# Performance work log

Hardware: AMD Instinct MI355X
Metric: run time of the kernel (lower is better)

## Reference

```python
import jax, jax.numpy as jnp
import numpy as np

# ---- constants derived exactly as in CQCCExtractor.__init__ ----
SR = 16000
FMIN = 32.7
N_BINS = 96
BINS_OCT = 24
N_CQCC = 20
HOP = 128
Q = 1.0 / (2.0 ** (1.0 / BINS_OCT) - 1.0)
MIN_WIN = max(16, int(Q * SR / FMIN))          # 16699
N_FFT = 1
while N_FFT < MIN_WIN * 2:
    N_FFT <<= 1                                # 65536
NUM_FREQ = N_FFT // 2 + 1                      # 32769


def _dct_mat():
    k = np.arange(N_CQCC)[:, None]
    n = np.arange(N_BINS)[None, :]
    return jnp.asarray(np.cos(np.pi * k * (2 * n + 1) / (2 * N_BINS)), dtype=jnp.float32)


def _delta(feat, N=2):
    # vectorized version of the per-frame python loop: d[t] = sum_n n*(f[min(t+n,T-1)] - f[max(t-n,0)]) / denom
    denom = 2 * sum(i * i for i in range(1, N + 1))
    T = feat.shape[0]
    p = jnp.concatenate([jnp.repeat(feat[:1], N, axis=0), feat, jnp.repeat(feat[-1:], N, axis=0)], axis=0)
    num = sum(n * (p[N + n:N + n + T] - p[N - n:N - n + T]) for n in range(1, N + 1))
    return num / denom


def setup_inputs() -> dict:
    key = jax.random.key(0)
    wav = jax.random.normal(key, (262144,), dtype=jnp.float32)
    return {"wav": wav}


def reference(wav) -> jnp.ndarray:
    # periodic hann window of length MIN_WIN, zero-padded (centered) to N_FFT like torch.stft
    w = 0.5 - 0.5 * jnp.cos(2.0 * jnp.pi * jnp.arange(MIN_WIN, dtype=jnp.float32) / MIN_WIN)
    left = (N_FFT - MIN_WIN) // 2
    win = jnp.zeros((N_FFT,), dtype=jnp.float32).at[left:left + MIN_WIN].set(w)

    # torch.stft(center=True, pad_mode='reflect')
    pad = N_FFT // 2
    x = jnp.pad(wav, pad, mode='reflect')
    n_frames = 1 + wav.shape[0] // HOP
    starts = jnp.arange(n_frames) * HOP
    frames = x[starts[:, None] + jnp.arange(N_FFT)[None, :]] * win      # [T, n_fft]
    spec = jnp.fft.rfft(frames, axis=-1)                                 # [T, F] complex64
    power = jnp.abs(spec) ** 2                                           # [T, F]

    # linear interpolation of STFT power at geometrically spaced CQT freqs
    cqt_freqs = FMIN * 2.0 ** (jnp.arange(N_BINS, dtype=jnp.float32) / BINS_OCT)
    idx_float = cqt_freqs / (SR / 2) * (NUM_FREQ - 1)
    idx_lo = jnp.clip(idx_float.astype(jnp.int32), 0, NUM_FREQ - 2)
    idx_hi = idx_lo + 1
    alpha = (idx_float - idx_lo.astype(jnp.float32))                     # [n_bins]
    cqt_power = (1.0 - alpha) * power[:, idx_lo] + alpha * power[:, idx_hi]  # [T, n_bins]

    log_cqt = jnp.log(jnp.maximum(cqt_power, 1e-8))
    cqcc = log_cqt @ _dct_mat().T                                        # [T, n_cqcc]
    # normalize over time (torch.std default is unbiased, ddof=1)
    cqcc = (cqcc - cqcc.mean(axis=0)) / (jnp.std(cqcc, axis=0, ddof=1) + 1e-8)

    d1 = _delta(cqcc)
    d2 = _delta(d1)
    return jnp.concatenate([cqcc, d1, d2], axis=-1)                      # [T, 3*n_cqcc]
```

## Files before the change

### kernel.cpp

```cpp
#include <hip/hip_runtime.h>
#include <math.h>

#define WAV_N     262144
#define HOP       128
#define MIN_WIN   16699
#define LEFT      24418
#define T_FRAMES  2049
#define N_BINS    96
#define N_CQCC    20
#define F_COMP    192
#define NF        576
#define NBLK      2179
#define NBP       2240
#define PARTLEN   59
#define FULLBLK   130
#define XS_VALID  278843

#define BT 64
#define FT 32
#define ASTRIDE 68

#define WS_QFP  0
#define WS_SC   20643840
#define WS_CQ   23801856
#define WS_SUMS 23965776
#define SCP     2056

__device__ __forceinline__ void f_to_fi_sigma(int f, int& fi, int& sigma) {
    int plane = f / 192;
    int c = f - plane * 192;
    int bin = c >> 1, hi = c & 1;
    float e    = (float)bin / 24.0f;
    float fb   = 32.7f * exp2f(e);
    float idxf = fb / 8000.0f * 32768.0f;
    fi = (int)idxf + hi;
    sigma = (plane == 0) ? 0 : (plane == 1 ? 1 : -1);
}

__global__ __launch_bounds__(256) void k_chunk(const float* __restrict__ wav,
                                               float4* __restrict__ QFP) {
    __shared__ float A_lds[128 * ASTRIDE];
    __shared__ __align__(16) float4 E_lds[128 * 16];
    int tid = threadIdx.x;
    int b0 = blockIdx.x * BT;
    int f0 = blockIdx.y * FT;

    {
        int sbase = 128 * b0;
        #pragma unroll
        for (int i = 0; i < 32; ++i) {
            int m = i * 256 + tid;
            int s = sbase + m;
            float v = 0.0f;
            if (s < XS_VALID) {
                int j = s - 8350;
                if (j < 0) j = -j;
                if (j >= WAV_N) j = 2 * WAV_N - 2 - j;
                v = wav[j];
            }
            A_lds[(m & 127) * ASTRIDE + (m >> 7)] = v;
        }
    }
    {
        #pragma unroll
        for (int i = 0; i < 8; ++i) {
            int ii = i * 256 + tid;
            int j = ii >> 4, ftp = ii & 15;
            float4 ev;
            #pragma unroll
            for (int half = 0; half < 2; ++half) {
                int f = f0 + 2 * ftp + half;
                int fi, sg; f_to_fi_sigma(f, fi, sg);
                float fr = (float)((j * fi) & 65535) * (1.0f / 65536.0f)
                         - (float)sg * (float)j * (1.0f / (float)MIN_WIN);
                fr -= rintf(fr);
                float sn, cs;
                __sincosf(6.283185307179586f * fr, &sn, &cs);
                if (half == 0) { ev.x = cs; ev.y = -sn; }
                else           { ev.z = cs; ev.w = -sn; }
            }
            E_lds[ii] = ev;
        }
    }
    __syncthreads();

    int ftp = tid & 15;
    int bg  = tid >> 4;
    float xr0[4] = {0,0,0,0}, xi0[4] = {0,0,0,0};
    float xr1[4] = {0,0,0,0}, xi1[4] = {0,0,0,0};
    float pr0[4], pi0[4], pr1[4], pi1[4];

    #pragma unroll 4
    for (int j = 0; j < PARTLEN; ++j) {
        float4 ev = E_lds[j * 16 + ftp];
        float4 a  = *(const float4*)&A_lds[j * ASTRIDE + bg * 4];
        const float aa[4] = {a.x, a.y, a.z, a.w};
        #pragma unroll
        for (int i = 0; i < 4; ++i) {
            xr0[i] = fmaf(aa[i], ev.x, xr0[i]); xi0[i] = fmaf(aa[i], ev.y, xi0[i]);
            xr1[i] = fmaf(aa[i], ev.z, xr1[i]); xi1[i] = fmaf(aa[i], ev.w, xi1[i]);
        }
    }
    #pragma unroll
    for (int i = 0; i < 4; ++i) {
        pr0[i] = xr0[i]; pi0[i] = xi0[i]; pr1[i] = xr1[i]; pi1[i] = xi1[i];
    }
    #pragma unroll 4
    for (int j = PARTLEN; j < 128; ++j) {
        float4 ev = E_lds[j * 16 + ftp];
        float4 a  = *(const float4*)&A_lds[j * ASTRIDE + bg * 4];
        const float aa[4] = {a.x, a.y, a.z, a.w};
        #pragma unroll
        for (int i = 0; i < 4; ++i) {
            xr0[i] = fmaf(aa[i], ev.x, xr0[i]); xi0[i] = fmaf(aa[i], ev.y, xi0[i]);
            xr1[i] = fmaf(aa[i], ev.z, xr1[i]); xi1[i] = fmaf(aa[i], ev.w, xi1[i]);
        }
    }

    int bBase = b0 + bg * 4;
    #pragma unroll
    for (int half = 0; half < 2; ++half) {
        int f = f0 + 2 * ftp + half;
        int fi, sg; f_to_fi_sigma(f, fi, sg);
        float4* dst = QFP + (size_t)f * NBP + bBase;
        #pragma unroll
        for (int i = 0; i < 4; ++i) {
            int b = bBase + i;
            unsigned ph = ((unsigned)fi * (unsigned)(LEFT + 128 * b)) & 65535u;
            float frf = (float)ph * (1.0f / 65536.0f)
                      - (float)sg * (float)((128 * b) % MIN_WIN) * (1.0f / (float)MIN_WIN);
            frf -= rintf(frf);
            float sn, cs;
            __sincosf(6.283185307179586f * frf, &sn, &cs);
            float fr_ = half ? xr1[i] : xr0[i], fi_ = half ? xi1[i] : xi0[i];
            float gr_ = half ? pr1[i] : pr0[i], gi_ = half ? pi1[i] : pi0[i];
            dst[i] = make_float4(fr_ * cs + fi_ * sn, fi_ * cs - fr_ * sn,
                                 gr_ * cs + gi_ * sn, gi_ * cs - gr_ * sn);
        }
    }
}

#define SEG 9
__global__ __launch_bounds__(256) void k_scan(const float4* __restrict__ QFP,
                                              float2* __restrict__ Sc,
                                              double* __restrict__ sums) {
    __shared__ float4 col[NBLK];
    __shared__ float2 acc[T_FRAMES];
    __shared__ double2 wsum[4];
    int tid = threadIdx.x;
    int c = blockIdx.x;
    if (c == 0 && tid < 40) sums[tid] = 0.0;

    for (int plane = 0; plane < 3; ++plane) {
        int f = plane * 192 + c;
        const float4* g = QFP + (size_t)f * NBP;
        #pragma unroll
        for (int k = 0; k < SEG; ++k) {
            int idx = k * 256 + tid;
            if (idx < NBLK) col[idx] = g[idx];
        }
        __syncthreads();
        int s0 = tid * SEG, s1 = min(s0 + SEG, NBLK);
        double sr = 0.0, si = 0.0;
        for (int i = s0; i < s1; ++i) { sr += col[i].x; si += col[i].y; }
        double r = sr, im = si;
        #pragma unroll
        for (int off = 1; off < 64; off <<= 1) {
            double pr = __shfl_up(r, off);
            double pi = __shfl_up(im, off);
            if ((tid & 63) >= off) { r += pr; im += pi; }
        }
        if ((tid & 63) == 63) wsum[tid >> 6] = make_double2(r, im);
        __syncthreads();
        double basr = 0.0, basi = 0.0;
        int w = tid >> 6;
        for (int ww = 0; ww < w; ++ww) { basr += wsum[ww].x; basi += wsum[ww].y; }
        double gr = basr + r - sr, gi = basi + im - si;
        for (int i = s0; i < s1; ++i) {
            float qx = col[i].x, qy = col[i].y;
            col[i].x = (float)gr; col[i].y = (float)gi;
            gr += qx; gi += qy;
        }
        __syncthreads();
        int fi_, sg_; f_to_fi_sigma(f, fi_, sg_);
        #pragma unroll
        for (int k = 0; k < SEG; ++k) {
            int t = k * 256 + tid;
            if (t < T_FRAMES) {
                float4 ca = col[t];
                float4 cb = col[t + FULLBLK];
                float ur = cb.x - ca.x + cb.z;
                float ui = cb.y - ca.y + cb.w;
                unsigned ph = ((unsigned)fi_ * 128u * (unsigned)t) & 65535u;
                float frf = (float)ph * (1.0f / 65536.0f)
                          - (float)sg_ * (float)((128 * t) % MIN_WIN) * (1.0f / (float)MIN_WIN);
                frf -= rintf(frf);
                float sn, cs;
                __sincosf(6.283185307179586f * frf, &sn, &cs);
                float vr = ur * cs - ui * sn;
                float vi = ur * sn + ui * cs;
                if (plane == 0) acc[t] = make_float2(0.5f * vr, 0.5f * vi);
                else { acc[t].x -= 0.25f * vr; acc[t].y -= 0.25f * vi; }
            }
        }
        __syncthreads();
    }
    #pragma unroll
    for (int k = 0; k < SEG; ++k) {
        int t = k * 256 + tid;
        if (t < T_FRAMES) Sc[(size_t)c * SCP + t] = acc[t];
    }
}

__global__ __launch_bounds__(256) void k_cqt(const float2* __restrict__ Sc,
                                             float* __restrict__ cq,
                                             double* __restrict__ sums) {
    __shared__ float dctm[N_CQCC * N_BINS];
    __shared__ float lg[8][N_BINS];
    __shared__ float cqv[8][N_CQCC];
    int tid = threadIdx.x;
    int tb = blockIdx.x * 8;
    for (int idx = tid; idx < N_CQCC * N_BINS; idx += 256) {
        int k = idx / N_BINS, b = idx - k * N_BINS;
        dctm[idx] = cosf((float)M_PI * (float)(k * (2 * b + 1)) / 192.0f);
    }
    int lt = tid >> 5, lane = tid & 31;
    int t = tb + lt;
    #pragma unroll
    for (int bb = 0; bb < 3; ++bb) {
        int b = lane + 32 * bb;
        float lv = 0.0f;
        if (t < T_FRAMES) {
            float2 lo = Sc[(size_t)(2 * b) * SCP + t];
            float2 hi = Sc[(size_t)(2 * b + 1) * SCP + t];
            float pl = lo.x * lo.x + lo.y * lo.y;
            float ph = hi.x * hi.x + hi.y * hi.y;
            float e    = (float)b / 24.0f;
            float fb   = 32.7f * exp2f(e);
            float idxf = fb / 8000.0f * 32768.0f;
            float alpha = idxf - (float)((int)idxf);
            float p = (1.0f - alpha) * pl + alpha * ph;
            lv = logf(fmaxf(p, 1e-8f));
        }
        lg[lt][b] = lv;
    }
    __syncthreads();
    if (tid < 8 * N_CQCC) {
        int lt2 = tid / N_CQCC, k = tid - lt2 * N_CQCC;
        int t2 = tb + lt2;
        float s = 0.0f;
        #pragma unroll 4
        for (int b = 0; b < N_BINS; ++b) s += dctm[k * N_BINS + b] * lg[lt2][b];
        cqv[lt2][k] = (t2 < T_FRAMES) ? s : 0.0f;
        if (t2 < T_FRAMES) cq[t2 * N_CQCC + k] = s;
    }
    __syncthreads();
    if (tid < N_CQCC) {
        double s1 = 0.0, s2 = 0.0;
        #pragma unroll
        for (int lt2 = 0; lt2 < 8; ++lt2) {
            if (tb + lt2 < T_FRAMES) {
                double v = (double)cqv[lt2][tid];
                s1 += v; s2 += v * v;
            }
        }
        atomicAdd(&sums[tid], s1);
        atomicAdd(&sums[N_CQCC + tid], s2);
    }
}

__device__ __forceinline__ int clampT(int v) {
    return v < 0 ? 0 : (v > T_FRAMES - 1 ? T_FRAMES - 1 : v);
}

__global__ void k_final(const float* __restrict__ cq, const double* __restrict__ sums,
                        float* __restrict__ out) {
    int gid = blockIdx.x * blockDim.x + threadIdx.x;
    if (gid >= T_FRAMES * N_CQCC) return;
    int t = gid / N_CQCC;
    int k = gid - t * N_CQCC;
    double S1 = sums[k], S2 = sums[N_CQCC + k];
    double md = S1 / (double)T_FRAMES;
    double var = (S2 - S1 * md) / (double)(T_FRAMES - 1);
    double sd = sqrt(var > 0.0 ? var : 0.0);
    float m = (float)md;
    float iv = (float)(1.0 / (sd + 1e-8));
    float cv[9];
    #pragma unroll
    for (int j = 0; j < 9; ++j)
        cv[j] = (cq[clampT(t + j - 4) * N_CQCC + k] - m) * iv;
    float dv[5];
    #pragma unroll
    for (int o = -2; o <= 2; ++o) {
        int p = clampT(t + o);
        int h1 = clampT(p + 1) - t, l1 = clampT(p - 1) - t;
        int h2 = clampT(p + 2) - t, l2 = clampT(p - 2) - t;
        dv[o + 2] = ((cv[h1 + 4] - cv[l1 + 4]) + 2.0f * (cv[h2 + 4] - cv[l2 + 4])) * 0.1f;
    }
    out[t * 60 + k]      = cv[4];
    out[t * 60 + 20 + k] = dv[2];
    out[t * 60 + 40 + k] = (dv[3] - dv[1] + 2.0f * (dv[4] - dv[0])) * 0.1f;
}

extern "C" void kernel_launch(void* const* d_in, const int* in_sizes, int n_in,
                              void* d_out, int out_size, void* d_ws, size_t ws_size,
                              hipStream_t stream) {
    const float* wav = (const float*)d_in[0];
    float* out = (float*)d_out;
    char* ws = (char*)d_ws;
    float4* QFP  = (float4*)(ws + WS_QFP);
    float2* Sc   = (float2*)(ws + WS_SC);
    float*  cq   = (float*)(ws + WS_CQ);
    double* sums = (double*)(ws + WS_SUMS);

    k_chunk<<<dim3((NBLK + BT - 1) / BT, NF / FT), 256, 0, stream>>>(wav, QFP);
    k_scan<<<F_COMP, 256, 0, stream>>>(QFP, Sc, sums);
    k_cqt<<<(T_FRAMES + 7) / 8, 256, 0, stream>>>(Sc, cq, sums);
    k_final<<<(T_FRAMES * N_CQCC + 255) / 256, 256, 0, stream>>>(cq, sums, out);
}
```

Measured before the change: 125.0 us.

## Generate chunk twiddles by recurrence and stream samples through LDS in chunks

k_chunk no longer precomputes a table of complex exponentials in shared memory. Each thread now builds them in registers with a complex-rotation recurrence, reseeded with an exact sincos at the start of each 32-sample chunk. Samples are staged in 32-row chunks, and each thread now covers 8 blocks × 2 frequencies, with 64 frequencies per workgroup. The aim is to remove the E table's LDS reads and the sincos setup, raise FMA-per-load reuse and shrink LDS so occupancy can rise. In exchange it adds per-thread register pressure, extra barriers, and accumulated float error from the recurrence across up to 32 steps.

```diff
diff --git a/kernel.cpp b/kernel.cpp
--- a/kernel.cpp
+++ b/kernel.cpp
@@ -15,10 +15,12 @@
 #define PARTLEN   59
 #define FULLBLK   130
 #define XS_VALID  278843
-
-#define BT 64
-#define FT 32
-#define ASTRIDE 68
+#define TWOPI     6.283185307179586f
+
+#define BT   64
+#define FTW  64
+#define JC   32
+#define AST  68
 
 #define WS_QFP  0
 #define WS_SC   20643840
@@ -39,103 +41,102 @@
 
 __global__ __launch_bounds__(256) void k_chunk(const float* __restrict__ wav,
                                                float4* __restrict__ QFP) {
-    __shared__ float A_lds[128 * ASTRIDE];
-    __shared__ __align__(16) float4 E_lds[128 * 16];
+    __shared__ float A_lds[JC * AST];
     int tid = threadIdx.x;
     int b0 = blockIdx.x * BT;
-    int f0 = blockIdx.y * FT;
-
-    {
-        int sbase = 128 * b0;
-        #pragma unroll
-        for (int i = 0; i < 32; ++i) {
+    int f0 = blockIdx.y * FTW;
+    int ftp = tid & 31;
+    int bg  = tid >> 5;
+    int bb  = b0 + bg * 8;
+
+    int fi[2], sg[2];
+    f_to_fi_sigma(f0 + 2 * ftp,     fi[0], sg[0]);
+    f_to_fi_sigma(f0 + 2 * ftp + 1, fi[1], sg[1]);
+
+    float Dr[2], Di[2];
+    #pragma unroll
+    for (int h = 0; h < 2; ++h) {
+        float fr = (float)fi[h] * (1.0f / 65536.0f)
+                 - (float)sg[h] * (1.0f / (float)MIN_WIN);
+        fr -= rintf(fr);
+        float sn, cs; __sincosf(TWOPI * fr, &sn, &cs);
+        Dr[h] = cs; Di[h] = -sn;
+    }
+
+    float xr[2][8], xi[2][8], pr[2][8], pi[2][8];
+    #pragma unroll
+    for (int h = 0; h < 2; ++h)
+        #pragma unroll
+        for (int i = 0; i < 8; ++i) { xr[h][i] = 0.f; xi[h][i] = 0.f; }
+
+    for (int jc = 0; jc < 4; ++jc) {
+        int jbase = jc * JC;
+        __syncthreads();
+        #pragma unroll
+        for (int i = 0; i < 8; ++i) {
             int m = i * 256 + tid;
-            int s = sbase + m;
+            int j = m & 31, bl = m >> 5;
+            int s = 128 * (b0 + bl) + jbase + j;
             float v = 0.0f;
             if (s < XS_VALID) {
-                int j = s - 8350;
-                if (j < 0) j = -j;
-                if (j >= WAV_N) j = 2 * WAV_N - 2 - j;
-                v = wav[j];
-            }
-            A_lds[(m & 127) * ASTRIDE + (m >> 7)] = v;
-        }
-    }
-    {
+                int w = s - 8350;
+                if (w < 0) w = -w;
+                if (w >= WAV_N) w = 2 * WAV_N - 2 - w;
+                v = wav[w];
+            }
+            A_lds[j * AST + bl] = v;
+        }
+        __syncthreads();
+        float Wr[2], Wi[2];
+        #pragma unroll
+        for (int h = 0; h < 2; ++h) {
+            float fr = (float)((jbase * fi[h]) & 65535) * (1.0f / 65536.0f)
+                     - (float)sg[h] * (float)jbase * (1.0f / (float)MIN_WIN);
+            fr -= rintf(fr);
+            float sn, cs; __sincosf(TWOPI * fr, &sn, &cs);
+            Wr[h] = cs; Wi[h] = -sn;
+        }
+        #pragma unroll 8
+        for (int j32 = 0; j32 < JC; ++j32) {
+            if (jc == 1 && j32 == PARTLEN - 32) {
+                #pragma unroll
+                for (int h = 0; h < 2; ++h)
+                    #pragma unroll
+                    for (int i = 0; i < 8; ++i) { pr[h][i] = xr[h][i]; pi[h][i] = xi[h][i]; }
+            }
+            float4 a0 = *(const float4*)&A_lds[j32 * AST + bg * 8];
+            float4 a1 = *(const float4*)&A_lds[j32 * AST + bg * 8 + 4];
+            const float aa[8] = {a0.x, a0.y, a0.z, a0.w, a1.x, a1.y, a1.z, a1.w};
+            #pragma unroll
+            for (int h = 0; h < 2; ++h) {
+                float wr = Wr[h], wi = Wi[h];
+                #pragma unroll
+                for (int i = 0; i < 8; ++i) {
+                    xr[h][i] = fmaf(aa[i], wr, xr[h][i]);
+                    xi[h][i] = fmaf(aa[i], wi, xi[h][i]);
+                }
+                Wr[h] = wr * Dr[h] - wi * Di[h];
+                Wi[h] = wr * Di[h] + wi * Dr[h];
+            }
+        }
+    }
+
+    #pragma unroll
+    for (int h = 0; h < 2; ++h) {
+        int f = f0 + 2 * ftp + h;
+        float4* dst = QFP + (size_t)f * NBP + bb;
         #pragma unroll
         for (int i = 0; i < 8; ++i) {
-            int ii = i * 256 + tid;
-            int j = ii >> 4, ftp = ii & 15;
-            float4 ev;
-            #pragma unroll
-            for (int half = 0; half < 2; ++half) {
-                int f = f0 + 2 * ftp + half;
-                int fi, sg; f_to_fi_sigma(f, fi, sg);
-                float fr = (float)((j * fi) & 65535) * (1.0f / 65536.0f)
-                         - (float)sg * (float)j * (1.0f / (float)MIN_WIN);
-                fr -= rintf(fr);
-                float sn, cs;
-                __sincosf(6.283185307179586f * fr, &sn, &cs);
-                if (half == 0) { ev.x = cs; ev.y = -sn; }
-                else           { ev.z = cs; ev.w = -sn; }
-            }
-            E_lds[ii] = ev;
-        }
-    }
-    __syncthreads();
-
-    int ftp = tid & 15;
-    int bg  = tid >> 4;
-    float xr0[4] = {0,0,0,0}, xi0[4] = {0,0,0,0};
-    float xr1[4] = {0,0,0,0}, xi1[4] = {0,0,0,0};
-    float pr0[4], pi0[4], pr1[4], pi1[4];
-
-    #pragma unroll 4
-    for (int j = 0; j < PARTLEN; ++j) {
-        float4 ev = E_lds[j * 16 + ftp];
-        float4 a  = *(const float4*)&A_lds[j * ASTRIDE + bg * 4];
-        const float aa[4] = {a.x, a.y, a.z, a.w};
-        #pragma unroll
-        for (int i = 0; i < 4; ++i) {
-            xr0[i] = fmaf(aa[i], ev.x, xr0[i]); xi0[i] = fmaf(aa[i], ev.y, xi0[i]);
-            xr1[i] = fmaf(aa[i], ev.z, xr1[i]); xi1[i] = fmaf(aa[i], ev.w, xi1[i]);
-        }
-    }
-    #pragma unroll
-    for (int i = 0; i < 4; ++i) {
-        pr0[i] = xr0[i]; pi0[i] = xi0[i]; pr1[i] = xr1[i]; pi1[i] = xi1[i];
-    }
-    #pragma unroll 4
-    for (int j = PARTLEN; j < 128; ++j) {
-        float4 ev = E_lds[j * 16 + ftp];
-        float4 a  = *(const float4*)&A_lds[j * ASTRIDE + bg * 4];
-        const float aa[4] = {a.x, a.y, a.z, a.w};
-        #pragma unroll
-        for (int i = 0; i < 4; ++i) {
-            xr0[i] = fmaf(aa[i], ev.x, xr0[i]); xi0[i] = fmaf(aa[i], ev.y, xi0[i]);
-            xr1[i] = fmaf(aa[i], ev.z, xr1[i]); xi1[i] = fmaf(aa[i], ev.w, xi1[i]);
-        }
-    }
-
-    int bBase = b0 + bg * 4;
-    #pragma unroll
-    for (int half = 0; half < 2; ++half) {
-        int f = f0 + 2 * ftp + half;
-        int fi, sg; f_to_fi_sigma(f, fi, sg);
-        float4* dst = QFP + (size_t)f * NBP + bBase;
-        #pragma unroll
-        for (int i = 0; i < 4; ++i) {
-            int b = bBase + i;
-            unsigned ph = ((unsigned)fi * (unsigned)(LEFT + 128 * b)) & 65535u;
+            int b = bb + i;
+            unsigned ph = ((unsigned)fi[h] * (unsigned)(LEFT + 128 * b)) & 65535u;
             float frf = (float)ph * (1.0f / 65536.0f)
-                      - (float)sg * (float)((128 * b) % MIN_WIN) * (1.0f / (float)MIN_WIN);
+                      - (float)sg[h] * (float)((128 * b) % MIN_WIN) * (1.0f / (float)MIN_WIN);
             frf -= rintf(frf);
-            float sn, cs;
-            __sincosf(6.283185307179586f * frf, &sn, &cs);
-            float fr_ = half ? xr1[i] : xr0[i], fi_ = half ? xi1[i] : xi0[i];
-            float gr_ = half ? pr1[i] : pr0[i], gi_ = half ? pi1[i] : pi0[i];
-            dst[i] = make_float4(fr_ * cs + fi_ * sn, fi_ * cs - fr_ * sn,
-                                 gr_ * cs + gi_ * sn, gi_ * cs - gr_ * sn);
+            float sn, cs; __sincosf(TWOPI * frf, &sn, &cs);
+            dst[i] = make_float4(xr[h][i] * cs + xi[h][i] * sn,
+                                 xi[h][i] * cs - xr[h][i] * sn,
+                                 pr[h][i] * cs + pi[h][i] * sn,
+                                 pi[h][i] * cs - pr[h][i] * sn);
         }
     }
 }
@@ -166,9 +167,9 @@
         double r = sr, im = si;
         #pragma unroll
         for (int off = 1; off < 64; off <<= 1) {
-            double pr = __shfl_up(r, off);
-            double pi = __shfl_up(im, off);
-            if ((tid & 63) >= off) { r += pr; im += pi; }
+            double prx = __shfl_up(r, off);
+            double piy = __shfl_up(im, off);
+            if ((tid & 63) >= off) { r += prx; im += piy; }
         }
         if ((tid & 63) == 63) wsum[tid >> 6] = make_double2(r, im);
         __syncthreads();
@@ -196,7 +197,7 @@
                           - (float)sg_ * (float)((128 * t) % MIN_WIN) * (1.0f / (float)MIN_WIN);
                 frf -= rintf(frf);
                 float sn, cs;
-                __sincosf(6.283185307179586f * frf, &sn, &cs);
+                __sincosf(TWOPI * frf, &sn, &cs);
                 float vr = ur * cs - ui * sn;
                 float vi = ur * sn + ui * cs;
                 if (plane == 0) acc[t] = make_float2(0.5f * vr, 0.5f * vi);
@@ -313,7 +314,7 @@
     float*  cq   = (float*)(ws + WS_CQ);
     double* sums = (double*)(ws + WS_SUMS);
 
-    k_chunk<<<dim3((NBLK + BT - 1) / BT, NF / FT), 256, 0, stream>>>(wav, QFP);
+    k_chunk<<<dim3(NBP / BT, NF / FTW), 256, 0, stream>>>(wav, QFP);
     k_scan<<<F_COMP, 256, 0, stream>>>(QFP, Sc, sums);
     k_cqt<<<(T_FRAMES + 7) / 8, 256, 0, stream>>>(Sc, cq, sums);
     k_final<<<(T_FRAMES * N_CQCC + 255) / 256, 256, 0, stream>>>(cq, sums, out);
```

Result: faster. 120.8 us (-3.3%).
